# Optimization experiments

Hardware: AMD Instinct MI355X
Metric: run time of the kernel (lower is better)

Reference implementation:

```python
import jax, jax.numpy as jnp
import numpy as np

B, S, D, E, H = 4, 2048, 1024, 8, 4096

def setup_inputs() -> dict:
    key = jax.random.key(0)
    ks = jax.random.split(key, 7)
    scale_d = 1.0 / np.sqrt(D)
    scale_h = 1.0 / np.sqrt(H)
    return {
        "x": jax.random.normal(ks[0], (B, S, D), dtype=jnp.float32),
        "Wr": jax.random.uniform(ks[1], (D, E), jnp.float32, -scale_d, scale_d),
        "br": jnp.zeros((E,), jnp.float32),
        "W1": jax.random.uniform(ks[2], (E, D, H), jnp.float32, -scale_d, scale_d),
        "b1": jax.random.uniform(ks[3], (E, H), jnp.float32, -scale_d, scale_d),
        "W2": jax.random.uniform(ks[4], (E, H, D), jnp.float32, -scale_h, scale_h),
        "b2": jax.random.uniform(ks[5], (E, D), jnp.float32, -scale_h, scale_h),
    }

def reference(x, Wr, br, W1, b1, W2, b2):
    # Router: softmax then argmax (top-1). Note: original does NOT scale
    # expert output by the routing weight and never applies capacity drop.
    route_logits = jnp.einsum("bsd,de->bse", x, Wr) + br
    routing_weights = jax.nn.softmax(route_logits, axis=-1)
    selected_expert = jnp.argmax(routing_weights, axis=-1)  # [B, S] int

    num_experts = W1.shape[0]
    out = jnp.zeros_like(x)
    # Fixed small loop over experts (structurally distinct weight slices);
    # select-by-mask keeps shapes static under jit.
    for e in range(num_experts):
        h = jax.nn.gelu(jnp.einsum("bsd,dh->bsh", x, W1[e]) + b1[e], approximate=False)
        y = jnp.einsum("bsh,hd->bsd", h, W2[e]) + b2[e]
        out = jnp.where((selected_expert == e)[..., None], y, out)
    return out
```

## Files before the change

kernel.cpp:

```cpp
#include <hip/hip_runtime.h>
#include <math.h>

#define TOK   8192
#define DD    1024
#define EE    8
#define HH    4096
#define MAXROWS 9216
#define MAXMT 72

typedef unsigned short u16;
typedef unsigned int   u32;
typedef __bf16 bf16x8 __attribute__((ext_vector_type(8)));
typedef float  f32x16 __attribute__((ext_vector_type(16)));

__device__ __forceinline__ u16 f2bf(float f) {
  union { float f; u32 u; } v; v.f = f;
  u32 r = v.u + 0x7fffu + ((v.u >> 16) & 1u);
  return (u16)(r >> 16);
}

__device__ __forceinline__ void gload16(const void* g, void* l) {
  __builtin_amdgcn_global_load_lds(
      (const __attribute__((address_space(1))) void*)g,
      (__attribute__((address_space(3))) void*)l, 16, 0, 0);
}

__global__ void k_init(int* rowmap, int* counts, int* fill) {
  int i = blockIdx.x * 256 + threadIdx.x;
  if (i < MAXROWS) rowmap[i] = -1;
  if (blockIdx.x == 0 && threadIdx.x < EE) { counts[threadIdx.x] = 0; fill[threadIdx.x] = 0; }
}

__global__ __launch_bounds__(256)
void k_route(const float* __restrict__ x, const float* __restrict__ Wr,
             const float* __restrict__ br, int* __restrict__ eid,
             int* __restrict__ counts, u16* __restrict__ xb) {
  int t = blockIdx.x * 4 + (threadIdx.x >> 6);
  int lt = threadIdx.x & 63;
  const float4* xr = (const float4*)(x + (size_t)t * DD);
  u16* xbr = xb + (size_t)t * DD;
  const float4* wrp = (const float4*)Wr;
  float acc[EE];
  #pragma unroll
  for (int e = 0; e < EE; ++e) acc[e] = 0.f;
  #pragma unroll
  for (int i = 0; i < 4; ++i) {
    int d4 = lt + 64 * i;
    float4 v = xr[d4];
    u32 p0 = (u32)f2bf(v.x) | ((u32)f2bf(v.y) << 16);
    u32 p1 = (u32)f2bf(v.z) | ((u32)f2bf(v.w) << 16);
    ((uint2*)xbr)[d4] = make_uint2(p0, p1);
    float vv[4] = { v.x, v.y, v.z, v.w };
    #pragma unroll
    for (int dd = 0; dd < 4; ++dd) {
      float xv = vv[dd];
      float4 a = wrp[(size_t)(d4 * 4 + dd) * 2];
      float4 b = wrp[(size_t)(d4 * 4 + dd) * 2 + 1];
      acc[0] += xv * a.x; acc[1] += xv * a.y; acc[2] += xv * a.z; acc[3] += xv * a.w;
      acc[4] += xv * b.x; acc[5] += xv * b.y; acc[6] += xv * b.z; acc[7] += xv * b.w;
    }
  }
  #pragma unroll
  for (int e = 0; e < EE; ++e)
    #pragma unroll
    for (int off = 32; off > 0; off >>= 1) acc[e] += __shfl_down(acc[e], off);
  if (lt == 0) {
    float best = -1e30f; int be = 0;
    #pragma unroll
    for (int e = 0; e < EE; ++e) {
      float v = acc[e] + br[e];
      if (v > best) { best = v; be = e; }
    }
    eid[t] = be;
    atomicAdd(&counts[be], 1);
  }
}

__global__ void k_scan(const int* __restrict__ counts, int* __restrict__ poff) {
  if (threadIdx.x == 0) {
    int off = 0; poff[0] = 0;
    for (int e = 0; e < EE; ++e) { off += ((counts[e] + 127) >> 7) << 7; poff[e + 1] = off; }
  }
}

__global__ void k_fillmap(const int* __restrict__ eid, const int* __restrict__ poff,
                          int* __restrict__ fill, int* __restrict__ rowmap) {
  int t = blockIdx.x * 256 + threadIdx.x;
  if (t < TOK) {
    int e = eid[t];
    int pos = atomicAdd(&fill[e], 1);
    rowmap[poff[e] + pos] = t;
  }
}

__global__ __launch_bounds__(256)
void k_transpose(const float* __restrict__ W, u16* __restrict__ WT, int K, int N) {
  __shared__ float tile[32][33];
  int e = blockIdx.z;
  int n0 = blockIdx.x * 32, k0 = blockIdx.y * 32;
  const float* We = W + (size_t)e * K * N;
  u16* WTe = WT + (size_t)e * K * N;
  int tx = threadIdx.x & 31, ty = threadIdx.x >> 5;
  #pragma unroll
  for (int i = 0; i < 4; ++i)
    tile[ty + 8 * i][tx] = We[(size_t)(k0 + ty + 8 * i) * N + n0 + tx];
  __syncthreads();
  #pragma unroll
  for (int i = 0; i < 4; ++i)
    WTe[(size_t)(n0 + ty + 8 * i) * K + k0 + tx] = f2bf(tile[tx][ty + 8 * i]);
}

template <int KDIM, int NDIM, bool G2>
__global__ __launch_bounds__(256, 3)
void k_gemm(const u16* __restrict__ Abase, const u16* __restrict__ WT,
            const float* __restrict__ bias, const int* __restrict__ poff,
            const int* __restrict__ rowmap, u16* __restrict__ hout,
            float* __restrict__ yout) {
  const int mt = blockIdx.y;
  const int mbase = mt * 128;
  if (mbase >= poff[EE]) return;
  int e = 0;
  #pragma unroll
  for (int q = 1; q < EE; ++q) e += (mbase >= poff[q]) ? 1 : 0;

  const int nbase = blockIdx.x * 128;
  const int tid = threadIdx.x;
  const int w = tid >> 6;
  const int lt = tid & 63;
  const int wr = w >> 1, wc = w & 1;

  __shared__ u16 lsA[2][128 * 32];
  __shared__ u16 lsB[2][128 * 32];

  const int srow = lt >> 2;
  const int clog = (lt & 3) ^ (srow & 3);
  int ar0, ar1;
  if (G2) { ar0 = mbase + w * 16 + srow; ar1 = ar0 + 64; }
  else {
    ar0 = rowmap[mbase + w * 16 + srow];      if (ar0 < 0) ar0 = 0;
    ar1 = rowmap[mbase + 64 + w * 16 + srow]; if (ar1 < 0) ar1 = 0;
  }
  const u16* gA0 = Abase + (size_t)ar0 * KDIM + clog * 8;
  const u16* gA1 = Abase + (size_t)ar1 * KDIM + clog * 8;
  const u16* wte = WT + (size_t)e * NDIM * KDIM + (size_t)nbase * KDIM;
  const u16* gB0 = wte + (size_t)(w * 16 + srow) * KDIM + clog * 8;
  const u16* gB1 = wte + (size_t)(64 + w * 16 + srow) * KDIM + clog * 8;

  f32x16 acc[2][2] = {};

  #define STAGE(buf, koff)                                          \
    do {                                                            \
      gload16(gA0 + (koff), &lsA[buf][(w * 16) * 32]);              \
      gload16(gA1 + (koff), &lsA[buf][(64 + w * 16) * 32]);         \
      gload16(gB0 + (koff), &lsB[buf][(w * 16) * 32]);              \
      gload16(gB1 + (koff), &lsB[buf][(64 + w * 16) * 32]);         \
    } while (0)

  STAGE(0, 0);
  const int KT = KDIM / 32;
  for (int bk = 0; bk < KT; ++bk) {
    __syncthreads();
    if (bk + 1 < KT) STAGE((bk + 1) & 1, (bk + 1) * 32);
    const u16* A = lsA[bk & 1];
    const u16* B = lsB[bk & 1];
    #pragma unroll
    for (int s = 0; s < 2; ++s) {
      bf16x8 af[2], bg[2];
      #pragma unroll
      for (int i = 0; i < 2; ++i) {
        int row = wr * 64 + i * 32 + (lt & 31);
        int phys = (s * 2 + (lt >> 5)) ^ (row & 3);
        af[i] = *(const bf16x8*)&A[row * 32 + phys * 8];
      }
      #pragma unroll
      for (int j = 0; j < 2; ++j) {
        int nn = wc * 64 + j * 32 + (lt & 31);
        int phys = (s * 2 + (lt >> 5)) ^ (nn & 3);
        bg[j] = *(const bf16x8*)&B[nn * 32 + phys * 8];
      }
      #pragma unroll
      for (int i = 0; i < 2; ++i)
        #pragma unroll
        for (int j = 0; j < 2; ++j)
          acc[i][j] = __builtin_amdgcn_mfma_f32_32x32x16_bf16(af[i], bg[j], acc[i][j], 0, 0, 0);
    }
  }
  #undef STAGE

  float bv[2];
  #pragma unroll
  for (int j = 0; j < 2; ++j)
    bv[j] = bias[(size_t)e * NDIM + nbase + wc * 64 + j * 32 + (lt & 31)];

  #pragma unroll
  for (int i = 0; i < 2; ++i) {
    const int rbase = wr * 64 + i * 32 + 4 * (lt >> 5);
    #pragma unroll
    for (int r = 0; r < 16; ++r) {
      const int rl = rbase + (r & 3) + 8 * (r >> 2);
      const int grow = mbase + rl;
      if (G2) {
        int tok = rowmap[grow];
        if (tok >= 0) {
          float* yp = yout + (size_t)tok * NDIM + nbase + wc * 64 + (lt & 31);
          #pragma unroll
          for (int j = 0; j < 2; ++j) yp[j * 32] = acc[i][j][r] + bv[j];
        }
      } else {
        u16* hp = hout + (size_t)grow * NDIM + nbase + wc * 64 + (lt & 31);
        #pragma unroll
        for (int j = 0; j < 2; ++j) {
          float v = acc[i][j][r] + bv[j];
          v = 0.5f * v * (1.0f + erff(v * 0.70710678118654752f));
          hp[j * 32] = f2bf(v);
        }
      }
    }
  }
}

extern "C" void kernel_launch(void* const* d_in, const int* in_sizes, int n_in,
                              void* d_out, int out_size, void* d_ws, size_t ws_size,
                              hipStream_t stream) {
  const float* x  = (const float*)d_in[0];
  const float* Wr = (const float*)d_in[1];
  const float* br = (const float*)d_in[2];
  const float* W1 = (const float*)d_in[3];
  const float* b1 = (const float*)d_in[4];
  const float* W2 = (const float*)d_in[5];
  const float* b2 = (const float*)d_in[6];
  float* out = (float*)d_out;

  char* ws = (char*)d_ws;
  int* eid    = (int*)(ws + 0);
  int* counts = (int*)(ws + 32768);
  int* fill   = (int*)(ws + 32768 + 64);
  int* poff   = (int*)(ws + 32768 + 128);
  int* rowmap = (int*)(ws + 33024);
  u16* xbf    = (u16*)(ws + 69888);
  u16* w1t    = (u16*)(ws + 16847104);
  u16* w2t    = (u16*)(ws + 83955968);
  u16* hbuf   = (u16*)(ws + 151064832);

  k_init<<<MAXROWS / 256, 256, 0, stream>>>(rowmap, counts, fill);
  k_route<<<TOK / 4, 256, 0, stream>>>(x, Wr, br, eid, counts, xbf);
  k_scan<<<1, 64, 0, stream>>>(counts, poff);
  k_fillmap<<<TOK / 256, 256, 0, stream>>>(eid, poff, fill, rowmap);
  k_transpose<<<dim3(HH / 32, DD / 32, EE), 256, 0, stream>>>(W1, w1t, DD, HH);
  k_transpose<<<dim3(DD / 32, HH / 32, EE), 256, 0, stream>>>(W2, w2t, HH, DD);
  k_gemm<DD, HH, false><<<dim3(HH / 128, MAXMT), 256, 0, stream>>>(xbf, w1t, b1, poff, rowmap, hbuf, nullptr);
  k_gemm<HH, DD, true><<<dim3(DD / 128, MAXMT), 256, 0, stream>>>(hbuf, w2t, b2, poff, rowmap, nullptr, out);
}
```

Before: 725.3 us.

## Enlarge GEMM tiles to 256x256 with 4-stage LDS pipeline and vectorized transpose

Replaces the 128x128 double-buffered expert GEMM with a 256x256 tile, 512-thread, 4-deep global_load_lds pipeline. It uses 16x16x32 MFMAs with a larger per-wave accumulator, explicit vmcnt waits and setprio. Expert row padding grows to 256 to match the new tile. The weight transpose now uses float4 loads and 16-byte packed bf16 stores. The aim is more data reuse per LDS byte and better latency hiding, at the cost of 128KB dynamic LDS, more registers, lower occupancy, and more padded rows per expert.

```diff
diff --git a/kernel.cpp b/kernel.cpp
--- a/kernel.cpp
+++ b/kernel.cpp
@@ -5,13 +5,13 @@
 #define DD    1024
 #define EE    8
 #define HH    4096
-#define MAXROWS 9216
-#define MAXMT 72
+#define MAXROWS 10240
+#define MAXMT 40
 
 typedef unsigned short u16;
 typedef unsigned int   u32;
 typedef __bf16 bf16x8 __attribute__((ext_vector_type(8)));
-typedef float  f32x16 __attribute__((ext_vector_type(16)));
+typedef float  f32x4  __attribute__((ext_vector_type(4)));
 
 __device__ __forceinline__ u16 f2bf(float f) {
   union { float f; u32 u; } v; v.f = f;
@@ -79,7 +79,7 @@
 __global__ void k_scan(const int* __restrict__ counts, int* __restrict__ poff) {
   if (threadIdx.x == 0) {
     int off = 0; poff[0] = 0;
-    for (int e = 0; e < EE; ++e) { off += ((counts[e] + 127) >> 7) << 7; poff[e + 1] = off; }
+    for (int e = 0; e < EE; ++e) { off += ((counts[e] + 255) >> 8) << 8; poff[e + 1] = off; }
   }
 }
 
@@ -95,124 +95,144 @@
 
 __global__ __launch_bounds__(256)
 void k_transpose(const float* __restrict__ W, u16* __restrict__ WT, int K, int N) {
-  __shared__ float tile[32][33];
-  int e = blockIdx.z;
-  int n0 = blockIdx.x * 32, k0 = blockIdx.y * 32;
+  __shared__ float tile[64][33];
+  const int e = blockIdx.z;
+  const int n0 = blockIdx.x * 32, k0 = blockIdx.y * 64;
   const float* We = W + (size_t)e * K * N;
   u16* WTe = WT + (size_t)e * K * N;
-  int tx = threadIdx.x & 31, ty = threadIdx.x >> 5;
-  #pragma unroll
-  for (int i = 0; i < 4; ++i)
-    tile[ty + 8 * i][tx] = We[(size_t)(k0 + ty + 8 * i) * N + n0 + tx];
+  const int t = threadIdx.x;
+  const int kk = t >> 3, nn = (t & 7) * 4;
+  #pragma unroll
+  for (int i = 0; i < 2; ++i) {
+    const float4 v = *(const float4*)&We[(size_t)(k0 + kk + 32 * i) * N + n0 + nn];
+    tile[kk + 32 * i][nn]     = v.x;
+    tile[kk + 32 * i][nn + 1] = v.y;
+    tile[kk + 32 * i][nn + 2] = v.z;
+    tile[kk + 32 * i][nn + 3] = v.w;
+  }
   __syncthreads();
-  #pragma unroll
-  for (int i = 0; i < 4; ++i)
-    WTe[(size_t)(n0 + ty + 8 * i) * K + k0 + tx] = f2bf(tile[tx][ty + 8 * i]);
+  const int n = t >> 3, c = t & 7;
+  u32 p[4];
+  #pragma unroll
+  for (int j = 0; j < 4; ++j) {
+    u32 lo = f2bf(tile[c * 8 + 2 * j][n]);
+    u32 hi = f2bf(tile[c * 8 + 2 * j + 1][n]);
+    p[j] = lo | (hi << 16);
+  }
+  *(uint4*)&WTe[(size_t)(n0 + n) * K + k0 + c * 8] = make_uint4(p[0], p[1], p[2], p[3]);
 }
 
 template <int KDIM, int NDIM, bool G2>
-__global__ __launch_bounds__(256, 3)
+__global__ __launch_bounds__(512, 2)
 void k_gemm(const u16* __restrict__ Abase, const u16* __restrict__ WT,
             const float* __restrict__ bias, const int* __restrict__ poff,
             const int* __restrict__ rowmap, u16* __restrict__ hout,
             float* __restrict__ yout) {
+  extern __shared__ char lds[];
   const int mt = blockIdx.y;
-  const int mbase = mt * 128;
+  const int mbase = mt * 256;
   if (mbase >= poff[EE]) return;
   int e = 0;
   #pragma unroll
   for (int q = 1; q < EE; ++q) e += (mbase >= poff[q]) ? 1 : 0;
 
-  const int nbase = blockIdx.x * 128;
+  const int nbase = blockIdx.x * 256;
   const int tid = threadIdx.x;
-  const int w = tid >> 6;
   const int lt = tid & 63;
-  const int wr = w >> 1, wc = w & 1;
-
-  __shared__ u16 lsA[2][128 * 32];
-  __shared__ u16 lsB[2][128 * 32];
-
-  const int srow = lt >> 2;
-  const int clog = (lt & 3) ^ (srow & 3);
-  int ar0, ar1;
-  if (G2) { ar0 = mbase + w * 16 + srow; ar1 = ar0 + 64; }
+  const int wid = tid >> 6;
+  const int wr = wid >> 2, wc = wid & 3;
+
+  const int row0 = tid >> 2;
+  const int cl = (tid & 3) ^ ((tid >> 3) & 3);
+  int r0, r1;
+  if (G2) { r0 = mbase + row0; r1 = r0 + 128; }
   else {
-    ar0 = rowmap[mbase + w * 16 + srow];      if (ar0 < 0) ar0 = 0;
-    ar1 = rowmap[mbase + 64 + w * 16 + srow]; if (ar1 < 0) ar1 = 0;
-  }
-  const u16* gA0 = Abase + (size_t)ar0 * KDIM + clog * 8;
-  const u16* gA1 = Abase + (size_t)ar1 * KDIM + clog * 8;
+    r0 = rowmap[mbase + row0];       if (r0 < 0) r0 = 0;
+    r1 = rowmap[mbase + 128 + row0]; if (r1 < 0) r1 = 0;
+  }
+  const u16* gA0 = Abase + (size_t)r0 * KDIM + cl * 8;
+  const u16* gA1 = Abase + (size_t)r1 * KDIM + cl * 8;
   const u16* wte = WT + (size_t)e * NDIM * KDIM + (size_t)nbase * KDIM;
-  const u16* gB0 = wte + (size_t)(w * 16 + srow) * KDIM + clog * 8;
-  const u16* gB1 = wte + (size_t)(64 + w * 16 + srow) * KDIM + clog * 8;
-
-  f32x16 acc[2][2] = {};
-
-  #define STAGE(buf, koff)                                          \
-    do {                                                            \
-      gload16(gA0 + (koff), &lsA[buf][(w * 16) * 32]);              \
-      gload16(gA1 + (koff), &lsA[buf][(64 + w * 16) * 32]);         \
-      gload16(gB0 + (koff), &lsB[buf][(w * 16) * 32]);              \
-      gload16(gB1 + (koff), &lsB[buf][(64 + w * 16) * 32]);         \
-    } while (0)
-
-  STAGE(0, 0);
+  const u16* gB0 = wte + (size_t)row0 * KDIM + cl * 8;
+  const u16* gB1 = wte + (size_t)(128 + row0) * KDIM + cl * 8;
+
+  char* dA = lds + tid * 16;
+  char* dB = lds + 65536 + tid * 16;
+
+#define STAGE(B, T) do {                               \
+    const int ko = (T) * 32;                           \
+    gload16(gA0 + ko, dA + (B) * 16384);               \
+    gload16(gA1 + ko, dA + (B) * 16384 + 8192);        \
+    gload16(gB0 + ko, dB + (B) * 16384);               \
+    gload16(gB1 + ko, dB + (B) * 16384 + 8192);        \
+  } while (0)
+
+  const int cph = ((lt >> 4) ^ ((lt >> 1) & 3)) << 4;
+  const char* pA = lds + (wr * 128 + (lt & 15)) * 64 + cph;
+  const char* pB = lds + 65536 + (wc * 64 + (lt & 15)) * 64 + cph;
+
+  f32x4 acc[8][4] = {};
+
+#define GSTEP(T, B, WAITI, DOSTAGE) do {                                              \
+    asm volatile("s_waitcnt vmcnt(" WAITI ")\n\ts_barrier" ::: "memory");             \
+    if (DOSTAGE) STAGE(((B) + 3) & 3, (T) + 3);                                       \
+    bf16x8 af[8], bg[4];                                                              \
+    _Pragma("unroll")                                                                 \
+    for (int m = 0; m < 8; ++m) af[m] = *(const bf16x8*)(pA + (B) * 16384 + m * 1024);\
+    _Pragma("unroll")                                                                 \
+    for (int n = 0; n < 4; ++n) bg[n] = *(const bf16x8*)(pB + (B) * 16384 + n * 1024);\
+    __builtin_amdgcn_s_setprio(1);                                                    \
+    _Pragma("unroll")                                                                 \
+    for (int m = 0; m < 8; ++m)                                                       \
+      _Pragma("unroll")                                                               \
+      for (int n = 0; n < 4; ++n)                                                     \
+        acc[m][n] = __builtin_amdgcn_mfma_f32_16x16x32_bf16(af[m], bg[n], acc[m][n], 0, 0, 0); \
+    __builtin_amdgcn_s_setprio(0);                                                    \
+  } while (0)
+
+  STAGE(0, 0); STAGE(1, 1); STAGE(2, 2);
   const int KT = KDIM / 32;
-  for (int bk = 0; bk < KT; ++bk) {
-    __syncthreads();
-    if (bk + 1 < KT) STAGE((bk + 1) & 1, (bk + 1) * 32);
-    const u16* A = lsA[bk & 1];
-    const u16* B = lsB[bk & 1];
-    #pragma unroll
-    for (int s = 0; s < 2; ++s) {
-      bf16x8 af[2], bg[2];
-      #pragma unroll
-      for (int i = 0; i < 2; ++i) {
-        int row = wr * 64 + i * 32 + (lt & 31);
-        int phys = (s * 2 + (lt >> 5)) ^ (row & 3);
-        af[i] = *(const bf16x8*)&A[row * 32 + phys * 8];
-      }
-      #pragma unroll
-      for (int j = 0; j < 2; ++j) {
-        int nn = wc * 64 + j * 32 + (lt & 31);
-        int phys = (s * 2 + (lt >> 5)) ^ (nn & 3);
-        bg[j] = *(const bf16x8*)&B[nn * 32 + phys * 8];
-      }
-      #pragma unroll
-      for (int i = 0; i < 2; ++i)
-        #pragma unroll
-        for (int j = 0; j < 2; ++j)
-          acc[i][j] = __builtin_amdgcn_mfma_f32_32x32x16_bf16(af[i], bg[j], acc[i][j], 0, 0, 0);
-    }
-  }
-  #undef STAGE
-
-  float bv[2];
-  #pragma unroll
-  for (int j = 0; j < 2; ++j)
-    bv[j] = bias[(size_t)e * NDIM + nbase + wc * 64 + j * 32 + (lt & 31)];
-
-  #pragma unroll
-  for (int i = 0; i < 2; ++i) {
-    const int rbase = wr * 64 + i * 32 + 4 * (lt >> 5);
-    #pragma unroll
-    for (int r = 0; r < 16; ++r) {
-      const int rl = rbase + (r & 3) + 8 * (r >> 2);
-      const int grow = mbase + rl;
+  #pragma unroll 1
+  for (int kt = 0; kt < KT - 4; kt += 4) {
+    GSTEP(kt + 0, 0, "8", true);
+    GSTEP(kt + 1, 1, "8", true);
+    GSTEP(kt + 2, 2, "8", true);
+    GSTEP(kt + 3, 3, "8", true);
+  }
+  GSTEP(KT - 4, 0, "8", true);
+  GSTEP(KT - 3, 1, "8", false);
+  GSTEP(KT - 2, 2, "4", false);
+  GSTEP(KT - 1, 3, "0", false);
+#undef GSTEP
+#undef STAGE
+
+  const int cl16 = lt & 15, rq = (lt >> 4) * 4;
+  float bv[4];
+  #pragma unroll
+  for (int n = 0; n < 4; ++n)
+    bv[n] = bias[(size_t)e * NDIM + nbase + wc * 64 + n * 16 + cl16];
+
+  const int colb = nbase + wc * 64 + cl16;
+  #pragma unroll
+  for (int m = 0; m < 8; ++m) {
+    const int rb = mbase + wr * 128 + m * 16 + rq;
+    #pragma unroll
+    for (int r = 0; r < 4; ++r) {
+      const int grow = rb + r;
       if (G2) {
-        int tok = rowmap[grow];
+        const int tok = rowmap[grow];
         if (tok >= 0) {
-          float* yp = yout + (size_t)tok * NDIM + nbase + wc * 64 + (lt & 31);
+          float* yp = yout + (size_t)tok * NDIM + colb;
           #pragma unroll
-          for (int j = 0; j < 2; ++j) yp[j * 32] = acc[i][j][r] + bv[j];
+          for (int n = 0; n < 4; ++n) yp[n * 16] = acc[m][n][r] + bv[n];
         }
       } else {
-        u16* hp = hout + (size_t)grow * NDIM + nbase + wc * 64 + (lt & 31);
+        u16* hp = hout + (size_t)grow * NDIM + colb;
         #pragma unroll
-        for (int j = 0; j < 2; ++j) {
-          float v = acc[i][j][r] + bv[j];
+        for (int n = 0; n < 4; ++n) {
+          float v = acc[m][n][r] + bv[n];
           v = 0.5f * v * (1.0f + erff(v * 0.70710678118654752f));
-          hp[j * 32] = f2bf(v);
+          hp[n * 16] = f2bf(v);
         }
       }
     }
@@ -234,20 +254,25 @@
   char* ws = (char*)d_ws;
   int* eid    = (int*)(ws + 0);
   int* counts = (int*)(ws + 32768);
-  int* fill   = (int*)(ws + 32768 + 64);
-  int* poff   = (int*)(ws + 32768 + 128);
+  int* fill   = (int*)(ws + 32832);
+  int* poff   = (int*)(ws + 32896);
   int* rowmap = (int*)(ws + 33024);
-  u16* xbf    = (u16*)(ws + 69888);
-  u16* w1t    = (u16*)(ws + 16847104);
-  u16* w2t    = (u16*)(ws + 83955968);
-  u16* hbuf   = (u16*)(ws + 151064832);
+  u16* xbf    = (u16*)(ws + 73984);
+  u16* w1t    = (u16*)(ws + 16851200);
+  u16* w2t    = (u16*)(ws + 83960064);
+  u16* hbuf   = (u16*)(ws + 151068928);
+
+  hipFuncSetAttribute((const void*)k_gemm<DD, HH, false>,
+                      hipFuncAttributeMaxDynamicSharedMemorySize, 131072);
+  hipFuncSetAttribute((const void*)k_gemm<HH, DD, true>,
+                      hipFuncAttributeMaxDynamicSharedMemorySize, 131072);
 
   k_init<<<MAXROWS / 256, 256, 0, stream>>>(rowmap, counts, fill);
   k_route<<<TOK / 4, 256, 0, stream>>>(x, Wr, br, eid, counts, xbf);
   k_scan<<<1, 64, 0, stream>>>(counts, poff);
   k_fillmap<<<TOK / 256, 256, 0, stream>>>(eid, poff, fill, rowmap);
-  k_transpose<<<dim3(HH / 32, DD / 32, EE), 256, 0, stream>>>(W1, w1t, DD, HH);
-  k_transpose<<<dim3(DD / 32, HH / 32, EE), 256, 0, stream>>>(W2, w2t, HH, DD);
-  k_gemm<DD, HH, false><<<dim3(HH / 128, MAXMT), 256, 0, stream>>>(xbf, w1t, b1, poff, rowmap, hbuf, nullptr);
-  k_gemm<HH, DD, true><<<dim3(DD / 128, MAXMT), 256, 0, stream>>>(hbuf, w2t, b2, poff, rowmap, nullptr, out);
-}
+  k_transpose<<<dim3(HH / 32, DD / 64, EE), 256, 0, stream>>>(W1, w1t, DD, HH);
+  k_transpose<<<dim3(DD / 32, HH / 64, EE), 256, 0, stream>>>(W2, w2t, HH, DD);
+  k_gemm<DD, HH, false><<<dim3(HH / 256, MAXMT), 512, 131072, stream>>>(xbf, w1t, b1, poff, rowmap, hbuf, nullptr);
+  k_gemm<HH, DD, true><<<dim3(DD / 256, MAXMT), 512, 131072, stream>>>(hbuf, w2t, b2, poff, rowmap, nullptr, out);
+}
```

New measurement: 692.1 us. 1.05x faster.
